# Performance work log

Hardware: AMD Instinct MI355X
Metric: run time of the kernel (lower is better)

Reference implementation:

```python
import jax, jax.numpy as jnp
import numpy as np

V = 50000   # vocab_size
D = 128     # emb_dim
HID = 64    # hidden_dim
HEADS = 4   # gat_heads
N = 20000   # n_nodes
E = 320000  # n_edges
SLOPE = 0.2 # PyG GATConv leaky_relu negative_slope


def setup_inputs() -> dict:
    key = jax.random.key(0)
    ks = jax.random.split(key, 13)
    nrm = lambda k, shp: jax.random.normal(k, shp, jnp.float32) * 0.1
    return {
        "node_idxs": jax.random.randint(ks[0], (N,), 0, V),
        "edge_index": jax.random.randint(ks[1], (2, E), 0, N),
        "emb": nrm(ks[2], (V, D)),
        # GAT layer 1: in=D, out=HID per head, HEADS heads, concat
        "W1": nrm(ks[3], (D, HEADS * HID)),
        "att_src1": nrm(ks[4], (HEADS, HID)),
        "att_dst1": nrm(ks[5], (HEADS, HID)),
        "b1": jnp.zeros((HEADS * HID,), jnp.float32),
        # GAT layer 2: in=HEADS*HID, out=HID, 1 head
        "W2": nrm(ks[6], (HEADS * HID, HID)),
        "att_src2": nrm(ks[7], (1, HID)),
        "att_dst2": nrm(ks[8], (1, HID)),
        "b2": jnp.zeros((HID,), jnp.float32),
        # attentional pooling gate MLP: Linear(HID,HID) -> ReLU -> Linear(HID,1)
        "gate_W1": nrm(ks[9], (HID, HID)),
        "gate_b1": jnp.zeros((HID,), jnp.float32),
        "gate_W2": nrm(ks[10], (HID, 1)),
        "gate_b2": jnp.zeros((1,), jnp.float32),
    }


def _segment_softmax(logits, seg, num_segments):
    # numerically stable softmax over edges grouped by destination node
    m = jax.ops.segment_max(logits, seg, num_segments=num_segments)
    e = jnp.exp(logits - m[seg])
    s = jax.ops.segment_sum(e, seg, num_segments=num_segments)
    return e / s[seg]


def _gat_layer(x, src, dst, n, W, a_src, a_dst, b, heads, ch):
    h = (x @ W).reshape(n, heads, ch)                 # [N,H,C]
    alpha_src = jnp.einsum('nhc,hc->nh', h, a_src)    # [N,H]
    alpha_dst = jnp.einsum('nhc,hc->nh', h, a_dst)    # [N,H]
    logits = jax.nn.leaky_relu(alpha_src[src] + alpha_dst[dst], SLOPE)  # [E,H]
    alpha = _segment_softmax(logits, dst, n)          # [E,H]
    out = jax.ops.segment_sum(h[src] * alpha[..., None], dst, num_segments=n)  # [N,H,C]
    return out.reshape(n, heads * ch) + b


def reference(node_idxs, edge_index, emb, W1, att_src1, att_dst1, b1,
              W2, att_src2, att_dst2, b2, gate_W1, gate_b1, gate_W2, gate_b2):
    n = node_idxs.shape[0]
    # PyG GATConv default add_self_loops=True
    loops = jnp.arange(n)
    src = jnp.concatenate([edge_index[0], loops])
    dst = jnp.concatenate([edge_index[1], loops])

    x = emb[node_idxs]                                                  # [N,D]
    x = jax.nn.elu(_gat_layer(x, src, dst, n, W1, att_src1, att_dst1, b1, HEADS, HID))
    x = jax.nn.elu(_gat_layer(x, src, dst, n, W2, att_src2, att_dst2, b2, 1, HID))

    # AttentionalAggregation with index=zeros -> global softmax-gated pool
    gate = jax.nn.relu(x @ gate_W1 + gate_b1) @ gate_W2 + gate_b2       # [N,1]
    w = jax.nn.softmax(gate, axis=0)
    return jnp.sum(w * x, axis=0, keepdims=True)                        # [1,HID]
```

## Files before the change

kernel.cpp:

```cpp
#include <hip/hip_runtime.h>

typedef float v4 __attribute__((ext_vector_type(4)));
typedef float v2 __attribute__((ext_vector_type(2)));

__device__ __forceinline__ float leaky(float x) { return x >= 0.f ? x : 0.2f * x; }
__device__ __forceinline__ float elu(float x) { return x > 0.f ? x : expm1f(x); }

#define WAVE_DRAIN() do { \
    asm volatile("s_waitcnt lgkmcnt(0)" ::: "memory"); \
    __builtin_amdgcn_wave_barrier(); \
  } while (0)

#define BCAP 64

__global__ __launch_bounds__(256) void k_init(
    const float* __restrict__ W1, const float* __restrict__ asv,
    const float* __restrict__ adv, float* __restrict__ uv,
    int* __restrict__ cnt, int* __restrict__ counter,
    float* __restrict__ accg, int nN) {
  int i = blockIdx.x * 256 + threadIdx.x;
  if (i < 512) {
    int k = i >> 2, h = i & 3;
    const float* w = &W1[(size_t)k * 256 + h * 64];
    const float* a = &asv[h * 64];
    const float* d = &adv[h * 64];
    float su = 0.f, sv = 0.f;
    #pragma unroll 8
    for (int c = 0; c < 64; ++c) { float x = w[c]; su += x * a[c]; sv += x * d[c]; }
    uv[k * 8 + h]     = su;
    uv[k * 8 + 4 + h] = sv;
  }
  if (i < nN) cnt[i] = 0;
  int j = i - nN;
  if (j >= 0 && j < 1280) accg[j] = 0.f;
  if (j == 1280) *counter = 0;
}

__global__ __launch_bounds__(256) void k_scatterattn(
    const int* __restrict__ ei, int* __restrict__ cnt, int* __restrict__ srtb,
    const int* __restrict__ nidx, const float* __restrict__ emb,
    const float* __restrict__ uv, float* __restrict__ as1,
    float* __restrict__ ad1, float* __restrict__ x,
    int nE, int eT, int eb, int nN) {
  int bid = blockIdx.x, t = threadIdx.x;
  if (bid < eb) {
    int e = bid * 256 + t;
    if (e >= eT) return;
    int s, d;
    if (e < nE) { s = ei[e]; d = ei[nE + e]; } else { s = d = e - nE; }
    int pos = atomicAdd(&cnt[d], 1);
    if (pos < BCAP) srtb[(size_t)d * BCAP + pos] = s;
  } else {
    int wv = t >> 6, lane = t & 63;
    int n = (bid - eb) * 4 + wv;
    if (n >= nN) return;
    const float* xp = &emb[(size_t)nidx[n] * 128];
    v2 xv = *(const v2*)&xp[lane * 2];
    *(v2*)&x[(size_t)n * 128 + lane * 2] = xv;
    v4 u0 = *(const v4*)&uv[(lane * 2) * 8];
    v4 d0 = *(const v4*)&uv[(lane * 2) * 8 + 4];
    v4 u1 = *(const v4*)&uv[(lane * 2 + 1) * 8];
    v4 d1 = *(const v4*)&uv[(lane * 2 + 1) * 8 + 4];
    v4 ps = u0 * xv[0] + u1 * xv[1];
    v4 pd = d0 * xv[0] + d1 * xv[1];
    for (int o = 32; o; o >>= 1) {
      ps[0] += __shfl_xor(ps[0], o); ps[1] += __shfl_xor(ps[1], o);
      ps[2] += __shfl_xor(ps[2], o); ps[3] += __shfl_xor(ps[3], o);
      pd[0] += __shfl_xor(pd[0], o); pd[1] += __shfl_xor(pd[1], o);
      pd[2] += __shfl_xor(pd[2], o); pd[3] += __shfl_xor(pd[3], o);
    }
    if (lane == 0) {
      *(v4*)&as1[(size_t)n * 4] = ps;
      *(v4*)&ad1[(size_t)n * 4] = pd;
    }
  }
}

__global__ __launch_bounds__(256) void k_aggx(
    const float* __restrict__ x,
    const float* __restrict__ as1, const float* __restrict__ ad1,
    const int* __restrict__ cnt, const int* __restrict__ srtb,
    float* __restrict__ g, int nN) {
  __shared__ int   ss[4][64];
  __shared__ __align__(16) float sw[4][256];
  int t = threadIdx.x;
  int wv = t >> 6, lane = t & 63;
  int n = blockIdx.x * 4 + wv;
  if (n >= nN) return;
  int c = cnt[n]; if (c > BCAP) c = BCAP;
  const int* sp = &srtb[(size_t)n * BCAP];
  v4 adn = *(const v4*)&ad1[(size_t)n * 4];
  int grp = lane >> 5;
  int c4  = (lane & 31) * 4;
  v4 a0 = (v4)(0.f), a1 = (v4)(0.f), a2 = (v4)(0.f), a3 = (v4)(0.f);
  v4 dn4 = (v4)(0.f);
  for (int base = 0; base < c; base += 64) {
    int m = c - base; if (m > 64) m = 64;
    WAVE_DRAIN();
    {
      int row = 0;
      v4 w4 = (v4)(0.f);
      if (lane < m) {
        int s = sp[base + lane];
        row = s;
        v4 a = *(const v4*)&as1[(size_t)s * 4];
        w4[0] = __expf(leaky(a[0] + adn[0]));
        w4[1] = __expf(leaky(a[1] + adn[1]));
        w4[2] = __expf(leaky(a[2] + adn[2]));
        w4[3] = __expf(leaky(a[3] + adn[3]));
      }
      ss[wv][lane] = row;
      *(v4*)&sw[wv][lane * 4] = w4;
    }
    WAVE_DRAIN();
    int mq = (m + 1) & ~1;
    #pragma unroll 4
    for (int j = 0; j < mq; j += 2) {
      int r = ss[wv][j + grp];
      v4 w4 = *(const v4*)&sw[wv][(j + grp) * 4];
      v4 xv = *(const v4*)&x[(size_t)r * 128 + c4];
      a0 += w4[0] * xv;
      a1 += w4[1] * xv;
      a2 += w4[2] * xv;
      a3 += w4[3] * xv;
      dn4 += w4;
    }
  }
  a0[0] += __shfl_xor(a0[0], 32); a0[1] += __shfl_xor(a0[1], 32);
  a0[2] += __shfl_xor(a0[2], 32); a0[3] += __shfl_xor(a0[3], 32);
  a1[0] += __shfl_xor(a1[0], 32); a1[1] += __shfl_xor(a1[1], 32);
  a1[2] += __shfl_xor(a1[2], 32); a1[3] += __shfl_xor(a1[3], 32);
  a2[0] += __shfl_xor(a2[0], 32); a2[1] += __shfl_xor(a2[1], 32);
  a2[2] += __shfl_xor(a2[2], 32); a2[3] += __shfl_xor(a2[3], 32);
  a3[0] += __shfl_xor(a3[0], 32); a3[1] += __shfl_xor(a3[1], 32);
  a3[2] += __shfl_xor(a3[2], 32); a3[3] += __shfl_xor(a3[3], 32);
  dn4[0] += __shfl_xor(dn4[0], 32); dn4[1] += __shfl_xor(dn4[1], 32);
  dn4[2] += __shfl_xor(dn4[2], 32); dn4[3] += __shfl_xor(dn4[3], 32);
  int hb = grp * 2;
  v4 lo = grp ? a2 : a0;
  v4 hi = grp ? a3 : a1;
  float ilo = 1.f / dn4[hb];
  float ihi = 1.f / dn4[hb + 1];
  size_t gb = (size_t)n * 512 + c4;
  *(v4*)&g[gb + (size_t)hb * 128]       = lo * ilo;
  *(v4*)&g[gb + (size_t)(hb + 1) * 128] = hi * ihi;
}

__global__ __launch_bounds__(256) void k_gemm1b(
    const float* __restrict__ g, const float* __restrict__ W1,
    const float* __restrict__ b1, float* __restrict__ x2, int nN) {
  __shared__ __align__(16) float xs[64 * 68];
  __shared__ __align__(16) float Ws[64 * 64];
  int t = threadIdx.x;
  int nbase = (blockIdx.x >> 2) * 64;
  int head  = blockIdx.x & 3;
  int cbase = head * 64;
  int c0 = (t & 15) * 4;
  int n0 = (t >> 4) * 4;
  float acc[4][4];
  for (int i = 0; i < 4; ++i) for (int j = 0; j < 4; ++j) acc[i][j] = 0.f;
  v4 z = (v4)(0.f);
  for (int kc = 0; kc < 2; ++kc) {
    __syncthreads();
    {
      int sn = t >> 2;
      int node = nbase + sn;
      int kp = (t & 3) * 16;
      bool v = node < nN;
      const float* sp = &g[(size_t)(v ? node : nN - 1) * 512 + head * 128 + kc * 64 + kp];
      v4 q0 = v ? *(const v4*)(sp + 0)  : z;
      v4 q1 = v ? *(const v4*)(sp + 4)  : z;
      v4 q2 = v ? *(const v4*)(sp + 8)  : z;
      v4 q3 = v ? *(const v4*)(sp + 12) : z;
      *(v4*)&xs[sn * 68 + kp + 0]  = q0;
      *(v4*)&xs[sn * 68 + kp + 4]  = q1;
      *(v4*)&xs[sn * 68 + kp + 8]  = q2;
      *(v4*)&xs[sn * 68 + kp + 12] = q3;
    }
    {
      int kk = t >> 2;
      int cp = (t & 3) * 16;
      const float* wp = &W1[(size_t)(kc * 64 + kk) * 256 + cbase + cp];
      v4 w0 = *(const v4*)(wp + 0);
      v4 w1 = *(const v4*)(wp + 4);
      v4 w2 = *(const v4*)(wp + 8);
      v4 w3 = *(const v4*)(wp + 12);
      *(v4*)&Ws[kk * 64 + cp + 0]  = w0;
      *(v4*)&Ws[kk * 64 + cp + 4]  = w1;
      *(v4*)&Ws[kk * 64 + cp + 8]  = w2;
      *(v4*)&Ws[kk * 64 + cp + 12] = w3;
    }
    __syncthreads();
    #pragma unroll 4
    for (int kk = 0; kk < 64; kk += 4) {
      v4 xv[4], wv[4];
      for (int i = 0; i < 4; ++i) xv[i] = *(const v4*)&xs[(n0 + i) * 68 + kk];
      for (int j = 0; j < 4; ++j) wv[j] = *(const v4*)&Ws[(kk + j) * 64 + c0];
      for (int i = 0; i < 4; ++i)
        for (int j = 0; j < 4; ++j) {
          float xd = xv[i][j];
          acc[i][0] += xd * wv[j][0];
          acc[i][1] += xd * wv[j][1];
          acc[i][2] += xd * wv[j][2];
          acc[i][3] += xd * wv[j][3];
        }
    }
  }
  v4 bb = *(const v4*)&b1[cbase + c0];
  for (int i = 0; i < 4; ++i) {
    int node = nbase + n0 + i;
    if (node < nN) {
      v4 o;
      o[0] = elu(acc[i][0] + bb[0]);
      o[1] = elu(acc[i][1] + bb[1]);
      o[2] = elu(acc[i][2] + bb[2]);
      o[3] = elu(acc[i][3] + bb[3]);
      *(v4*)&x2[(size_t)node * 256 + cbase + c0] = o;
    }
  }
}

__global__ __launch_bounds__(256) void k_gemm2(
    const float* __restrict__ x2, const float* __restrict__ W2,
    const float* __restrict__ asv, const float* __restrict__ adv,
    float* __restrict__ h2, float* __restrict__ as2, float* __restrict__ ad2, int nN) {
  __shared__ __align__(16) float xs[64 * 68];
  __shared__ __align__(16) float Ws[64 * 64];
  int t = threadIdx.x;
  int nbase = blockIdx.x * 64;
  int c0 = (t & 15) * 4;
  int n0 = (t >> 4) * 4;
  float acc[4][4];
  for (int i = 0; i < 4; ++i) for (int j = 0; j < 4; ++j) acc[i][j] = 0.f;
  v4 z = (v4)(0.f);
  for (int kc = 0; kc < 4; ++kc) {
    __syncthreads();
    {
      int sn = t >> 2;
      int node = nbase + sn;
      int kp = (t & 3) * 16;
      bool v = node < nN;
      const float* sp = &x2[(size_t)(v ? node : nN - 1) * 256 + kc * 64 + kp];
      v4 q0 = v ? *(const v4*)(sp + 0)  : z;
      v4 q1 = v ? *(const v4*)(sp + 4)  : z;
      v4 q2 = v ? *(const v4*)(sp + 8)  : z;
      v4 q3 = v ? *(const v4*)(sp + 12) : z;
      *(v4*)&xs[sn * 68 + kp + 0]  = q0;
      *(v4*)&xs[sn * 68 + kp + 4]  = q1;
      *(v4*)&xs[sn * 68 + kp + 8]  = q2;
      *(v4*)&xs[sn * 68 + kp + 12] = q3;
    }
    {
      int kk = t >> 2;
      int cp = (t & 3) * 16;
      const float* wp = &W2[(size_t)(kc * 64 + kk) * 64 + cp];
      v4 w0 = *(const v4*)(wp + 0);
      v4 w1 = *(const v4*)(wp + 4);
      v4 w2 = *(const v4*)(wp + 8);
      v4 w3 = *(const v4*)(wp + 12);
      *(v4*)&Ws[kk * 64 + cp + 0]  = w0;
      *(v4*)&Ws[kk * 64 + cp + 4]  = w1;
      *(v4*)&Ws[kk * 64 + cp + 8]  = w2;
      *(v4*)&Ws[kk * 64 + cp + 12] = w3;
    }
    __syncthreads();
    #pragma unroll 4
    for (int kk = 0; kk < 64; kk += 4) {
      v4 xv[4], wv[4];
      for (int i = 0; i < 4; ++i) xv[i] = *(const v4*)&xs[(n0 + i) * 68 + kk];
      for (int j = 0; j < 4; ++j) wv[j] = *(const v4*)&Ws[(kk + j) * 64 + c0];
      for (int i = 0; i < 4; ++i)
        for (int j = 0; j < 4; ++j) {
          float xd = xv[i][j];
          acc[i][0] += xd * wv[j][0];
          acc[i][1] += xd * wv[j][1];
          acc[i][2] += xd * wv[j][2];
          acc[i][3] += xd * wv[j][3];
        }
    }
  }
  v4 asl = *(const v4*)&asv[c0];
  v4 adl = *(const v4*)&adv[c0];
  for (int i = 0; i < 4; ++i) {
    int node = nbase + n0 + i;
    v4 o; o[0] = acc[i][0]; o[1] = acc[i][1]; o[2] = acc[i][2]; o[3] = acc[i][3];
    float ps = o[0]*asl[0] + o[1]*asl[1] + o[2]*asl[2] + o[3]*asl[3];
    float pd = o[0]*adl[0] + o[1]*adl[1] + o[2]*adl[2] + o[3]*adl[3];
    ps += __shfl_xor(ps, 1); pd += __shfl_xor(pd, 1);
    ps += __shfl_xor(ps, 2); pd += __shfl_xor(pd, 2);
    ps += __shfl_xor(ps, 4); pd += __shfl_xor(pd, 4);
    ps += __shfl_xor(ps, 8); pd += __shfl_xor(pd, 8);
    if (node < nN) {
      *(v4*)&h2[(size_t)node * 64 + c0] = o;
      if ((t & 15) == 0) { as2[node] = ps; ad2[node] = pd; }
    }
  }
}

__global__ __launch_bounds__(256) void k_agg2gate(
    const float* __restrict__ h2, const float* __restrict__ as2,
    const float* __restrict__ ad2, const float* __restrict__ b2,
    const int* __restrict__ cnt, const int* __restrict__ srtb,
    const float* __restrict__ gW1, const float* __restrict__ gb1,
    const float* __restrict__ gW2, const float* __restrict__ gb2,
    float* __restrict__ acc_g, int* __restrict__ counter,
    float* __restrict__ out, int nN, int nBlk) {
  __shared__ __align__(16) float gwT[64 * 68];
  __shared__ int   ss[4][64];
  __shared__ float sw[4][64];
  __shared__ __align__(16) float xr[4][64];
  __shared__ float snum[4][64];
  __shared__ float sden[4];
  __shared__ int lastFlag;
  int t = threadIdx.x, bid = blockIdx.x;
  int wv = t >> 6, lane = t & 63;
  for (int i = t; i < 4096; i += 256) gwT[(i & 63) * 68 + (i >> 6)] = gW1[i];
  __syncthreads();
  const int grp = lane >> 4;
  const int c4  = (lane & 15) * 4;
  const int nwav = nBlk * 4;
  float gb1l = gb1[lane];
  float gw2l = gW2[lane];
  float gb2s = gb2[0];
  float num = 0.f, den = 0.f;
  for (int n = bid * 4 + wv; n < nN; n += nwav) {
    int c = cnt[n]; if (c > BCAP) c = BCAP;
    const int* sp = &srtb[(size_t)n * BCAP];
    float adn = ad2[n];
    v4 acc = (v4)(0.f);
    float dn = 0.f;
    for (int base = 0; base < c; base += 64) {
      int m = c - base; if (m > 64) m = 64;
      WAVE_DRAIN();
      {
        int s = 0; float ww = 0.f;
        if (lane < m) { s = sp[base + lane]; ww = __expf(leaky(as2[s] + adn)); }
        ss[wv][lane] = s;
        sw[wv][lane] = ww;
      }
      WAVE_DRAIN();
      int mq = (m + 3) & ~3;
      #pragma unroll 4
      for (int j = 0; j < mq; j += 4) {
        int s = ss[wv][j + grp];
        float wj = sw[wv][j + grp];
        v4 hv = *(const v4*)&h2[(size_t)s * 64 + c4];
        acc += wj * hv;
        dn += wj;
      }
    }
    acc[0] += __shfl_xor(acc[0], 16); acc[1] += __shfl_xor(acc[1], 16);
    acc[2] += __shfl_xor(acc[2], 16); acc[3] += __shfl_xor(acc[3], 16);
    dn += __shfl_xor(dn, 16);
    acc[0] += __shfl_xor(acc[0], 32); acc[1] += __shfl_xor(acc[1], 32);
    acc[2] += __shfl_xor(acc[2], 32); acc[3] += __shfl_xor(acc[3], 32);
    dn += __shfl_xor(dn, 32);
    WAVE_DRAIN();
    if (lane < 16) {
      float inv = 1.f / dn;
      v4 bb = *(const v4*)&b2[c4];
      v4 o;
      o[0] = elu(acc[0] * inv + bb[0]);
      o[1] = elu(acc[1] * inv + bb[1]);
      o[2] = elu(acc[2] * inv + bb[2]);
      o[3] = elu(acc[3] * inv + bb[3]);
      *(v4*)&xr[wv][c4] = o;
    }
    WAVE_DRAIN();
    float xv = xr[wv][lane];
    float hid = gb1l;
    for (int d4 = 0; d4 < 64; d4 += 4) {
      v4 xs4 = *(const v4*)&xr[wv][d4];
      v4 gv  = *(const v4*)&gwT[lane * 68 + d4];
      hid += xs4[0] * gv[0] + xs4[1] * gv[1] + xs4[2] * gv[2] + xs4[3] * gv[3];
    }
    hid = fmaxf(hid, 0.f);
    float p = hid * gw2l;
    for (int o = 32; o; o >>= 1) p += __shfl_xor(p, o);
    float gg = __expf(p + gb2s);
    num += gg * xv;
    den += gg;
  }
  snum[wv][lane] = num;
  if (lane == 0) sden[wv] = den;
  __syncthreads();
  float* myacc = acc_g + (size_t)(bid & 15) * 80;
  if (t < 64) {
    float s = 0.f;
    for (int k = 0; k < 4; ++k) s += snum[k][t];
    atomicAdd(&myacc[t], s);
  }
  if (t == 64) {
    float s = sden[0] + sden[1] + sden[2] + sden[3];
    atomicAdd(&myacc[64], s);
  }
  asm volatile("s_waitcnt vmcnt(0)" ::: "memory");
  __syncthreads();
  if (t == 0) {
    int ticket = atomicAdd(counter, 1);
    lastFlag = (ticket == nBlk - 1) ? 1 : 0;
  }
  __syncthreads();
  if (lastFlag && t < 64) {
    float s = 0.f, dn = 0.f;
    #pragma unroll
    for (int r = 0; r < 16; ++r) {
      s  += __hip_atomic_load(&acc_g[(size_t)r * 80 + t],  __ATOMIC_RELAXED, __HIP_MEMORY_SCOPE_AGENT);
      dn += __hip_atomic_load(&acc_g[(size_t)r * 80 + 64], __ATOMIC_RELAXED, __HIP_MEMORY_SCOPE_AGENT);
    }
    out[t] = s / dn;
  }
}

extern "C" void kernel_launch(void* const* d_in, const int* in_sizes, int n_in,
                              void* d_out, int out_size, void* d_ws, size_t ws_size,
                              hipStream_t stream) {
  const int*   nidx = (const int*)d_in[0];
  const int*   ei   = (const int*)d_in[1];
  const float* emb  = (const float*)d_in[2];
  const float* W1   = (const float*)d_in[3];
  const float* as1v = (const float*)d_in[4];
  const float* ad1v = (const float*)d_in[5];
  const float* b1   = (const float*)d_in[6];
  const float* W2   = (const float*)d_in[7];
  const float* as2v = (const float*)d_in[8];
  const float* ad2v = (const float*)d_in[9];
  const float* b2   = (const float*)d_in[10];
  const float* gW1  = (const float*)d_in[11];
  const float* gb1  = (const float*)d_in[12];
  const float* gW2  = (const float*)d_in[13];
  const float* gb2  = (const float*)d_in[14];
  float* out = (float*)d_out;

  const int nN = in_sizes[0];
  const int nE = in_sizes[1] / 2;
  const int eT = nE + nN;
  const int nb4 = (nN + 3) / 4;
  const int NB  = 1024;

  float* f = (float*)d_ws;
  size_t off = 0;
  float* g    = f + off; off += (size_t)nN * 512;
  float* x2   = f + off; off += (size_t)nN * 256;
  float* x    = f + off; off += (size_t)nN * 128;
  float* h2   = f + off; off += (size_t)nN * 64;
  float* as1  = f + off; off += (size_t)nN * 4;
  float* ad1  = f + off; off += (size_t)nN * 4;
  float* as2  = f + off; off += nN;
  float* ad2  = f + off; off += nN;
  float* uv   = f + off; off += 1024;
  float* accg = f + off; off += 16 * 80;
  int* cnt    = (int*)(f + off); off += nN;
  int* counter= (int*)(f + off); off += 1;
  int* srtb   = (int*)(f + off); off += (size_t)nN * BCAP;

  int ib = (nN + 1281 + 255) / 256;
  k_init       <<<ib, 256, 0, stream>>>(W1, as1v, ad1v, uv, cnt, counter, accg, nN);

  int eb = (eT + 255) / 256;
  k_scatterattn<<<eb + nb4, 256, 0, stream>>>(ei, cnt, srtb, nidx, emb, uv,
                                              as1, ad1, x, nE, eT, eb, nN);
  k_aggx       <<<nb4, 256, 0, stream>>>(x, as1, ad1, cnt, srtb, g, nN);

  int nt64 = (nN + 63) / 64;
  k_gemm1b     <<<nt64 * 4, 256, 0, stream>>>(g, W1, b1, x2, nN);
  k_gemm2      <<<nt64, 256, 0, stream>>>(x2, W2, as2v, ad2v, h2, as2, ad2, nN);

  k_agg2gate   <<<NB, 256, 0, stream>>>(h2, as2, ad2, b2, cnt, srtb,
                                        gW1, gb1, gW2, gb2, accg, counter,
                                        out, nN, NB);
}
```

Before: 232.8 us.

## Fuse layer-1 output GEMM and layer-2 GEMM into one kernel with split-K reduction

Merges the layer-1 projection/ELU GEMM and the layer-2 GEMM into a single 1024-thread kernel. Each of four 256-thread groups computes one head's 64-column slice, applies bias and ELU into shared memory, and multiplies by its 64-row slice of W2. The four partial products are then summed in shared memory before the attention logits are computed. This drops the 20000x256 x2 intermediate round-trip through global memory and one launch, at the cost of about 132KB of LDS per block (one block per CU) and far fewer blocks, which may leave CUs idle or cause a tail.

```diff
diff --git a/kernel.cpp b/kernel.cpp
--- a/kernel.cpp
+++ b/kernel.cpp
@@ -146,28 +146,32 @@
   *(v4*)&g[gb + (size_t)(hb + 1) * 128] = hi * ihi;
 }
 
-__global__ __launch_bounds__(256) void k_gemm1b(
+__global__ __launch_bounds__(1024) void k_gemmf12(
     const float* __restrict__ g, const float* __restrict__ W1,
-    const float* __restrict__ b1, float* __restrict__ x2, int nN) {
-  __shared__ __align__(16) float xs[64 * 68];
-  __shared__ __align__(16) float Ws[64 * 64];
+    const float* __restrict__ b1, const float* __restrict__ W2,
+    const float* __restrict__ asv, const float* __restrict__ adv,
+    float* __restrict__ h2, float* __restrict__ as2, float* __restrict__ ad2, int nN) {
+  extern __shared__ __align__(16) float sm[];
   int t = threadIdx.x;
-  int nbase = (blockIdx.x >> 2) * 64;
-  int head  = blockIdx.x & 3;
-  int cbase = head * 64;
-  int c0 = (t & 15) * 4;
-  int n0 = (t >> 4) * 4;
+  int hg = t >> 8;
+  int lt = t & 255;
+  float* xs = sm + (size_t)hg * 8448;
+  float* Ws = xs + 4352;
+  int nbase = blockIdx.x * 64;
+  int cbase = hg * 64;
+  int c0 = (lt & 15) * 4;
+  int n0 = (lt >> 4) * 4;
+  v4 z = (v4)(0.f);
   float acc[4][4];
   for (int i = 0; i < 4; ++i) for (int j = 0; j < 4; ++j) acc[i][j] = 0.f;
-  v4 z = (v4)(0.f);
   for (int kc = 0; kc < 2; ++kc) {
     __syncthreads();
     {
-      int sn = t >> 2;
+      int sn = lt >> 2;
       int node = nbase + sn;
-      int kp = (t & 3) * 16;
+      int kp = (lt & 3) * 16;
       bool v = node < nN;
-      const float* sp = &g[(size_t)(v ? node : nN - 1) * 512 + head * 128 + kc * 64 + kp];
+      const float* sp = &g[(size_t)(v ? node : nN - 1) * 512 + hg * 128 + kc * 64 + kp];
       v4 q0 = v ? *(const v4*)(sp + 0)  : z;
       v4 q1 = v ? *(const v4*)(sp + 4)  : z;
       v4 q2 = v ? *(const v4*)(sp + 8)  : z;
@@ -178,8 +182,8 @@
       *(v4*)&xs[sn * 68 + kp + 12] = q3;
     }
     {
-      int kk = t >> 2;
-      int cp = (t & 3) * 16;
+      int kk = lt >> 2;
+      int cp = (lt & 3) * 16;
       const float* wp = &W1[(size_t)(kc * 64 + kk) * 256 + cbase + cp];
       v4 w0 = *(const v4*)(wp + 0);
       v4 w1 = *(const v4*)(wp + 4);
@@ -206,93 +210,74 @@
         }
     }
   }
-  v4 bb = *(const v4*)&b1[cbase + c0];
-  for (int i = 0; i < 4; ++i) {
-    int node = nbase + n0 + i;
-    if (node < nN) {
+  __syncthreads();
+  {
+    v4 bb = *(const v4*)&b1[cbase + c0];
+    for (int i = 0; i < 4; ++i) {
       v4 o;
       o[0] = elu(acc[i][0] + bb[0]);
       o[1] = elu(acc[i][1] + bb[1]);
       o[2] = elu(acc[i][2] + bb[2]);
       o[3] = elu(acc[i][3] + bb[3]);
-      *(v4*)&x2[(size_t)node * 256 + cbase + c0] = o;
-    }
-  }
-}
-
-__global__ __launch_bounds__(256) void k_gemm2(
-    const float* __restrict__ x2, const float* __restrict__ W2,
-    const float* __restrict__ asv, const float* __restrict__ adv,
-    float* __restrict__ h2, float* __restrict__ as2, float* __restrict__ ad2, int nN) {
-  __shared__ __align__(16) float xs[64 * 68];
-  __shared__ __align__(16) float Ws[64 * 64];
-  int t = threadIdx.x;
-  int nbase = blockIdx.x * 64;
-  int c0 = (t & 15) * 4;
-  int n0 = (t >> 4) * 4;
-  float acc[4][4];
-  for (int i = 0; i < 4; ++i) for (int j = 0; j < 4; ++j) acc[i][j] = 0.f;
-  v4 z = (v4)(0.f);
-  for (int kc = 0; kc < 4; ++kc) {
-    __syncthreads();
-    {
-      int sn = t >> 2;
-      int node = nbase + sn;
-      int kp = (t & 3) * 16;
-      bool v = node < nN;
-      const float* sp = &x2[(size_t)(v ? node : nN - 1) * 256 + kc * 64 + kp];
-      v4 q0 = v ? *(const v4*)(sp + 0)  : z;
-      v4 q1 = v ? *(const v4*)(sp + 4)  : z;
-      v4 q2 = v ? *(const v4*)(sp + 8)  : z;
-      v4 q3 = v ? *(const v4*)(sp + 12) : z;
-      *(v4*)&xs[sn * 68 + kp + 0]  = q0;
-      *(v4*)&xs[sn * 68 + kp + 4]  = q1;
-      *(v4*)&xs[sn * 68 + kp + 8]  = q2;
-      *(v4*)&xs[sn * 68 + kp + 12] = q3;
-    }
-    {
-      int kk = t >> 2;
-      int cp = (t & 3) * 16;
-      const float* wp = &W2[(size_t)(kc * 64 + kk) * 64 + cp];
-      v4 w0 = *(const v4*)(wp + 0);
-      v4 w1 = *(const v4*)(wp + 4);
-      v4 w2 = *(const v4*)(wp + 8);
-      v4 w3 = *(const v4*)(wp + 12);
-      *(v4*)&Ws[kk * 64 + cp + 0]  = w0;
-      *(v4*)&Ws[kk * 64 + cp + 4]  = w1;
-      *(v4*)&Ws[kk * 64 + cp + 8]  = w2;
-      *(v4*)&Ws[kk * 64 + cp + 12] = w3;
-    }
-    __syncthreads();
-    #pragma unroll 4
-    for (int kk = 0; kk < 64; kk += 4) {
-      v4 xv[4], wv[4];
-      for (int i = 0; i < 4; ++i) xv[i] = *(const v4*)&xs[(n0 + i) * 68 + kk];
-      for (int j = 0; j < 4; ++j) wv[j] = *(const v4*)&Ws[(kk + j) * 64 + c0];
-      for (int i = 0; i < 4; ++i)
-        for (int j = 0; j < 4; ++j) {
-          float xd = xv[i][j];
-          acc[i][0] += xd * wv[j][0];
-          acc[i][1] += xd * wv[j][1];
-          acc[i][2] += xd * wv[j][2];
-          acc[i][3] += xd * wv[j][3];
-        }
-    }
-  }
-  v4 asl = *(const v4*)&asv[c0];
-  v4 adl = *(const v4*)&adv[c0];
-  for (int i = 0; i < 4; ++i) {
-    int node = nbase + n0 + i;
-    v4 o; o[0] = acc[i][0]; o[1] = acc[i][1]; o[2] = acc[i][2]; o[3] = acc[i][3];
-    float ps = o[0]*asl[0] + o[1]*asl[1] + o[2]*asl[2] + o[3]*asl[3];
-    float pd = o[0]*adl[0] + o[1]*adl[1] + o[2]*adl[2] + o[3]*adl[3];
-    ps += __shfl_xor(ps, 1); pd += __shfl_xor(pd, 1);
-    ps += __shfl_xor(ps, 2); pd += __shfl_xor(pd, 2);
-    ps += __shfl_xor(ps, 4); pd += __shfl_xor(pd, 4);
-    ps += __shfl_xor(ps, 8); pd += __shfl_xor(pd, 8);
-    if (node < nN) {
-      *(v4*)&h2[(size_t)node * 64 + c0] = o;
-      if ((t & 15) == 0) { as2[node] = ps; ad2[node] = pd; }
+      *(v4*)&xs[(n0 + i) * 68 + c0] = o;
+    }
+    int kk = lt >> 2;
+    int cp = (lt & 3) * 16;
+    const float* wp = &W2[(size_t)(cbase + kk) * 64 + cp];
+    v4 w0 = *(const v4*)(wp + 0);
+    v4 w1 = *(const v4*)(wp + 4);
+    v4 w2 = *(const v4*)(wp + 8);
+    v4 w3 = *(const v4*)(wp + 12);
+    *(v4*)&Ws[kk * 64 + cp + 0]  = w0;
+    *(v4*)&Ws[kk * 64 + cp + 4]  = w1;
+    *(v4*)&Ws[kk * 64 + cp + 8]  = w2;
+    *(v4*)&Ws[kk * 64 + cp + 12] = w3;
+  }
+  __syncthreads();
+  float acc2[4][4];
+  for (int i = 0; i < 4; ++i) for (int j = 0; j < 4; ++j) acc2[i][j] = 0.f;
+  #pragma unroll 4
+  for (int kk = 0; kk < 64; kk += 4) {
+    v4 xv[4], wv[4];
+    for (int i = 0; i < 4; ++i) xv[i] = *(const v4*)&xs[(n0 + i) * 68 + kk];
+    for (int j = 0; j < 4; ++j) wv[j] = *(const v4*)&Ws[(kk + j) * 64 + c0];
+    for (int i = 0; i < 4; ++i)
+      for (int j = 0; j < 4; ++j) {
+        float xd = xv[i][j];
+        acc2[i][0] += xd * wv[j][0];
+        acc2[i][1] += xd * wv[j][1];
+        acc2[i][2] += xd * wv[j][2];
+        acc2[i][3] += xd * wv[j][3];
+      }
+  }
+  __syncthreads();
+  for (int i = 0; i < 4; ++i)
+    *(v4*)&Ws[(n0 + i) * 64 + c0] = *(v4*)&acc2[i][0];
+  __syncthreads();
+  if (hg == 0) {
+    const float* p0 = sm + 4352;
+    const float* p1 = sm + 1 * 8448 + 4352;
+    const float* p2 = sm + 2 * 8448 + 4352;
+    const float* p3 = sm + 3 * 8448 + 4352;
+    v4 asl = *(const v4*)&asv[c0];
+    v4 adl = *(const v4*)&adv[c0];
+    for (int i = 0; i < 4; ++i) {
+      int node = nbase + n0 + i;
+      int ofs = (n0 + i) * 64 + c0;
+      v4 o = *(const v4*)&p0[ofs];
+      o += *(const v4*)&p1[ofs];
+      o += *(const v4*)&p2[ofs];
+      o += *(const v4*)&p3[ofs];
+      float ps = o[0]*asl[0] + o[1]*asl[1] + o[2]*asl[2] + o[3]*asl[3];
+      float pd = o[0]*adl[0] + o[1]*adl[1] + o[2]*adl[2] + o[3]*adl[3];
+      ps += __shfl_xor(ps, 1); pd += __shfl_xor(pd, 1);
+      ps += __shfl_xor(ps, 2); pd += __shfl_xor(pd, 2);
+      ps += __shfl_xor(ps, 4); pd += __shfl_xor(pd, 4);
+      ps += __shfl_xor(ps, 8); pd += __shfl_xor(pd, 8);
+      if (node < nN) {
+        *(v4*)&h2[(size_t)node * 64 + c0] = o;
+        if ((lt & 15) == 0) { as2[node] = ps; ad2[node] = pd; }
+      }
     }
   }
 }
@@ -441,7 +426,6 @@
   float* f = (float*)d_ws;
   size_t off = 0;
   float* g    = f + off; off += (size_t)nN * 512;
-  float* x2   = f + off; off += (size_t)nN * 256;
   float* x    = f + off; off += (size_t)nN * 128;
   float* h2   = f + off; off += (size_t)nN * 64;
   float* as1  = f + off; off += (size_t)nN * 4;
@@ -463,8 +447,8 @@
   k_aggx       <<<nb4, 256, 0, stream>>>(x, as1, ad1, cnt, srtb, g, nN);
 
   int nt64 = (nN + 63) / 64;
-  k_gemm1b     <<<nt64 * 4, 256, 0, stream>>>(g, W1, b1, x2, nN);
-  k_gemm2      <<<nt64, 256, 0, stream>>>(x2, W2, as2v, ad2v, h2, as2, ad2, nN);
+  k_gemmf12    <<<nt64, 1024, 135168, stream>>>(g, W1, b1, W2, as2v, ad2v,
+                                                h2, as2, ad2, nN);
 
   k_agg2gate   <<<NB, 256, 0, stream>>>(h2, as2, ad2, b2, cnt, srtb,
                                         gW1, gb1, gW2, gb2, accg, counter,
```

Measured after the change: 250.8 us. +7.7%, slower.
